# Kernel optimization log

Hardware: AMD Instinct MI355X
Metric: run time of the kernel (lower is better)

The kernel has to match this reference:

```python
import jax, jax.numpy as jnp
import numpy as np

B, T, C, H = 4, 2048, 1024, 16
HD = C // H  # head_dim = 64


def setup_inputs() -> dict:
    key = jax.random.key(0)
    k1, k2, k3 = jax.random.split(key, 3)
    x = jax.random.normal(k1, (B, T, C), dtype=jnp.float32)
    # nn.Linear weights are [out, in]; we store transposed [in, out] for x @ W
    w_qkv = jax.random.normal(k2, (C, 3 * C), dtype=jnp.float32) * (1.0 / np.sqrt(C))
    w_proj = jax.random.normal(k3, (C, C), dtype=jnp.float32) * (1.0 / np.sqrt(C))
    return {"x": x, "w_qkv": w_qkv, "w_proj": w_proj}


def reference(x, w_qkv, w_proj):
    Bs, Ts, Cs = x.shape
    qkv = x @ w_qkv  # [B,T,3C]
    q, k, v = jnp.split(qkv, 3, axis=-1)

    def split_heads(t):
        return t.reshape(Bs, Ts, H, HD).transpose(0, 2, 1, 3)  # [B,H,T,HD]

    q, k, v = split_heads(q), split_heads(k), split_heads(v)
    scale = 1.0 / np.sqrt(HD)
    scores = jnp.einsum('bhqd,bhkd->bhqk', q, k) * scale  # [B,H,T,T]
    causal = jnp.tril(jnp.ones((Ts, Ts), dtype=bool))
    scores = jnp.where(causal, scores, -jnp.inf)
    weights = jax.nn.softmax(scores, axis=-1)
    out = jnp.einsum('bhqk,bhkd->bhqd', weights, v)  # [B,H,T,HD]
    out = out.transpose(0, 2, 1, 3).reshape(Bs, Ts, Cs)
    return out @ w_proj
```

## Files before the change

kernel.cpp:

```cpp
#include <hip/hip_runtime.h>
#include <stdint.h>


typedef __attribute__((ext_vector_type(8))) short bf16x8;
typedef __attribute__((ext_vector_type(4))) float f32x4;

#define MFMA(a, b, c) __builtin_amdgcn_mfma_f32_16x16x32_bf16((a), (b), (c), 0, 0, 0)

#define NB 4
#define NT 2048
#define NC 1024
#define NH 16
#define HD 64
#define SCALE_Q 0.18033688011112042f

__device__ __forceinline__ short f2bf(float f) {
  union { float fv; uint32_t u; } v; v.fv = f;
  uint32_t u = v.u;
  uint32_t r = (u + 0x7fffu + ((u >> 16) & 1u)) >> 16;
  return (short)(r & 0xffffu);
}

__device__ __forceinline__ void gl_lds16(const void* g, void* l) {
  __builtin_amdgcn_global_load_lds(
      (const __attribute__((address_space(1))) void*)g,
      (__attribute__((address_space(3))) void*)l, 16, 0, 0);
}


__global__ void cast_f32_bf16(const float* __restrict__ src, short* __restrict__ dst, int n8) {
  int i = blockIdx.x * blockDim.x + threadIdx.x;
  if (i >= n8) return;
  const float4* s4 = (const float4*)src;
  float4 a = s4[2 * i], b = s4[2 * i + 1];
  bf16x8 o;
  o[0] = f2bf(a.x); o[1] = f2bf(a.y); o[2] = f2bf(a.z); o[3] = f2bf(a.w);
  o[4] = f2bf(b.x); o[5] = f2bf(b.y); o[6] = f2bf(b.z); o[7] = f2bf(b.w);
  *(bf16x8*)&dst[8 * i] = o;
}

__global__ void transpose_cast(const float* __restrict__ src, short* __restrict__ dst,
                               int R, int Cc) {
  __shared__ float tile[64][65];
  int tid = threadIdx.x;
  int c0 = blockIdx.x * 64;
  int r0 = blockIdx.y * 64;
  int lr = tid >> 4;
  int lc = (tid & 15) * 4;
#pragma unroll
  for (int i = 0; i < 4; i++) {
    int rr = lr + i * 16;
    float4 v = *(const float4*)&src[(size_t)(r0 + rr) * Cc + c0 + lc];
    tile[rr][lc + 0] = v.x; tile[rr][lc + 1] = v.y;
    tile[rr][lc + 2] = v.z; tile[rr][lc + 3] = v.w;
  }
  __syncthreads();
  int oc = tid >> 2;
  int seg = (tid & 3) * 16;
  bf16x8 o0, o1;
#pragma unroll
  for (int u = 0; u < 8; u++) o0[u] = f2bf(tile[seg + u][oc]);
#pragma unroll
  for (int u = 0; u < 8; u++) o1[u] = f2bf(tile[seg + 8 + u][oc]);
  size_t base = (size_t)(c0 + oc) * R + r0 + seg;
  *(bf16x8*)&dst[base] = o0;
  *(bf16x8*)&dst[base + 8] = o1;
}


__global__ __launch_bounds__(256, 2)
void gemm_bt_kernel(const short* __restrict__ A, const short* __restrict__ BT,
                    int N, int K, int mode,
                    short* __restrict__ q, short* __restrict__ kk, short* __restrict__ vT,
                    float* __restrict__ f_out) {
  __shared__ short sA[128 * 32];
  __shared__ short sB[128 * 32];
  const int tid = threadIdx.x;
  const int lane = tid & 63;
  const int w = tid >> 6;
  const int quad = lane >> 4;
  const int r = lane & 15;
  const int bn0 = blockIdx.x * 128;
  const int bm0 = blockIdx.y * 128;
  const int wm = (w >> 1) * 64;
  const int wn = (w & 1) * 64;

  f32x4 acc[4][4];
#pragma unroll
  for (int i = 0; i < 4; i++)
#pragma unroll
    for (int j = 0; j < 4; j++) acc[i][j] = (f32x4){0.f, 0.f, 0.f, 0.f};

  for (int kb = 0; kb < K; kb += 32) {
    __syncthreads();
#pragma unroll
    for (int rnd = 0; rnd < 2; rnd++) {
      int ci = rnd * 256 + tid;
      int m = ci >> 2, inner = ci & 3;
      const char* ga = (const char*)(A + (size_t)(bm0 + m) * K + kb) + inner * 16;
      gl_lds16(ga, (char*)sA + ci * 16);
      const char* gb = (const char*)(BT + (size_t)(bn0 + m) * K + kb) + inner * 16;
      gl_lds16(gb, (char*)sB + ci * 16);
    }
    __syncthreads();
    bf16x8 af[4], bfr[4];
#pragma unroll
    for (int i = 0; i < 4; i++) {
      af[i]  = *(const bf16x8*)&sA[(wm + i * 16 + r) * 32 + quad * 8];
      bfr[i] = *(const bf16x8*)&sB[(wn + i * 16 + r) * 32 + quad * 8];
    }
#pragma unroll
    for (int i = 0; i < 4; i++)
#pragma unroll
      for (int j = 0; j < 4; j++)
        acc[i][j] = MFMA(af[i], bfr[j], acc[i][j]);
  }

  if (mode == 0) {
#pragma unroll
    for (int i = 0; i < 4; i++) {
      int mbase = bm0 + wm + i * 16 + quad * 4;
#pragma unroll
      for (int j = 0; j < 4; j++) {
        int n = bn0 + wn + j * 16 + r;
        int sel = n >> 10, rem = n & 1023, h = rem >> 6, d = rem & 63;
#pragma unroll
        for (int reg = 0; reg < 4; reg++) {
          int m = mbase + reg;
          int b = m >> 11, t = m & 2047;
          int bh = b * NH + h;
          float v = acc[i][j][reg];
          if (sel == 0) {
            q[((size_t)bh * NT + t) * HD + d] = f2bf(v * SCALE_Q);
          } else if (sel == 1) {
            kk[((size_t)bh * NT + t) * HD + d] = f2bf(v);
          } else {
            vT[((size_t)bh * HD + d) * NT + t] = f2bf(v);
          }
        }
      }
    }
  } else {
#pragma unroll
    for (int i = 0; i < 4; i++)
#pragma unroll
      for (int j = 0; j < 4; j++) {
        int n = bn0 + wn + j * 16 + r;
#pragma unroll
        for (int reg = 0; reg < 4; reg++) {
          int m = bm0 + wm + i * 16 + quad * 4 + reg;
          f_out[(size_t)m * N + n] = acc[i][j][reg];
        }
      }
  }
}


__global__ __launch_bounds__(256, 3)
void attn_kernel(const short* __restrict__ Q, const short* __restrict__ Kg,
                 const short* __restrict__ VT, short* __restrict__ Og) {
  __shared__ short sK[128 * 64];
  __shared__ short sV[64 * 128];
  __shared__ short sP[4][16 * 136];
  const int tid = threadIdx.x;
  const int lane = tid & 63;
  const int w = tid >> 6;
  const int quad = lane >> 4;
  const int r = lane & 15;

  const int n = blockIdx.x;
  const int xcd = n & 7;
  const int slot = n >> 3;
  const int bh = xcd * 8 + (slot & 7);
  const int band = 15 - (slot >> 3);
  const int ntile = band + 1;

  const short* Qb  = Q  + (size_t)bh * NT * HD;
  const short* Kb  = Kg + (size_t)bh * NT * HD;
  const short* VTb = VT + (size_t)bh * HD * NT;

  const int q0 = band * 128 + w * 32;

  bf16x8 bQ[2][2];
#pragma unroll
  for (int mi = 0; mi < 2; mi++) {
    const size_t qrow = ((size_t)q0 + mi * 16 + r) * HD;
    bQ[mi][0] = *(const bf16x8*)&Qb[qrow + quad * 8];
    bQ[mi][1] = *(const bf16x8*)&Qb[qrow + 32 + quad * 8];
  }
  bf16x8 vone;
#pragma unroll
  for (int u = 0; u < 8; u++) vone[u] = (short)0x3F80;

  f32x4 acc[2][4];
  f32x4 lacc[2];
#pragma unroll
  for (int mi = 0; mi < 2; mi++) {
    lacc[mi] = (f32x4){0.f, 0.f, 0.f, 0.f};
#pragma unroll
    for (int dt = 0; dt < 4; dt++) acc[mi][dt] = (f32x4){0.f, 0.f, 0.f, 0.f};
  }

  for (int kt = 0; kt < ntile; kt++) {
    const int kv0 = kt * 128;
    const bool diag = (kt == band);
    __syncthreads();
#pragma unroll
    for (int j = 0; j < 4; j++) {
      int idx = (w * 4 + j) * 64 + lane;
      int krow = idx >> 3, kch = idx & 7;
      int kg = kch ^ (krow & 7);
      gl_lds16(Kb + (size_t)(kv0 + krow) * HD + kg * 8, (char*)sK + idx * 16);
      int vrow = idx >> 4, vch = idx & 15;
      int vg = (vch & 8) | ((vch ^ vrow) & 7);
      gl_lds16(VTb + (size_t)vrow * NT + kv0 + vg * 8, (char*)sV + idx * 16);
    }
    __syncthreads();

    bf16x8 vf[4][4];
#pragma unroll
    for (int dt = 0; dt < 4; dt++)
#pragma unroll
      for (int c = 0; c < 4; c++) {
        int ch = quad + 4 * c;
        int sw = (ch & 8) | ((ch ^ (r & 7)) & 7);
        vf[dt][c] = *(const bf16x8*)&sV[(dt * 16 + r) * 128 + sw * 8];
      }

#pragma unroll
    for (int mi = 0; mi < 2; mi++) {
      const int nts = diag ? (w * 2 + mi + 1) : 8;
#pragma unroll
      for (int nt = 0; nt < 8; nt++) {
        uint32_t pk0 = 0, pk1 = 0;
        if (nt < nts) {
          const int krow = nt * 16 + r;
          const int sw0 = quad ^ (r & 7);
          bf16x8 k0 = *(const bf16x8*)&sK[krow * 64 + sw0 * 8];
          bf16x8 k1 = *(const bf16x8*)&sK[krow * 64 + (sw0 ^ 4) * 8];
          f32x4 st = (f32x4){0.f, 0.f, 0.f, 0.f};
          st = MFMA(k0, bQ[mi][0], st);
          st = MFMA(k1, bQ[mi][1], st);
          if (diag && nt == nts - 1) {
            const int kvb = kv0 + nt * 16 + quad * 4;
            const int qg = q0 + mi * 16 + r;
#pragma unroll
            for (int reg = 0; reg < 4; reg++)
              if (kvb + reg > qg) st[reg] = -1e30f;
          }
          uint32_t b0 = (uint16_t)f2bf(__builtin_amdgcn_exp2f(st[0]));
          uint32_t b1 = (uint16_t)f2bf(__builtin_amdgcn_exp2f(st[1]));
          uint32_t b2 = (uint16_t)f2bf(__builtin_amdgcn_exp2f(st[2]));
          uint32_t b3 = (uint16_t)f2bf(__builtin_amdgcn_exp2f(st[3]));
          pk0 = b0 | (b1 << 16);
          pk1 = b2 | (b3 << 16);
        }
        *(uint2*)&sP[w][r * 136 + nt * 16 + quad * 4] = make_uint2(pk0, pk1);
      }
      __builtin_amdgcn_s_waitcnt(0xc07f);
      bf16x8 aP[4];
#pragma unroll
      for (int c = 0; c < 4; c++)
        aP[c] = *(const bf16x8*)&sP[w][r * 136 + c * 32 + quad * 8];
#pragma unroll
      for (int c = 0; c < 4; c++)
        lacc[mi] = MFMA(aP[c], vone, lacc[mi]);
#pragma unroll
      for (int dt = 0; dt < 4; dt++)
#pragma unroll
        for (int c = 0; c < 4; c++)
          acc[mi][dt] = MFMA(aP[c], vf[dt][c], acc[mi][dt]);
    }
  }

  const int b = bh >> 4, h = bh & 15;
#pragma unroll
  for (int mi = 0; mi < 2; mi++)
#pragma unroll
    for (int reg = 0; reg < 4; reg++) {
      const int trow = q0 + mi * 16 + quad * 4 + reg;
      const float inv = 1.0f / lacc[mi][reg];
      const size_t base = ((size_t)(b * NT + trow)) * NC + h * HD;
#pragma unroll
      for (int dt = 0; dt < 4; dt++)
        Og[base + dt * 16 + r] = f2bf(acc[mi][dt][reg] * inv);
    }
}


extern "C" void kernel_launch(void* const* d_in, const int* in_sizes, int n_in,
                              void* d_out, int out_size, void* d_ws, size_t ws_size,
                              hipStream_t stream) {
  const float* x     = (const float*)d_in[0];
  const float* wqkv  = (const float*)d_in[1];
  const float* wproj = (const float*)d_in[2];
  float* out = (float*)d_out;

  char* ws = (char*)d_ws;
  short* xb  = (short*)(ws + 0);
  short* wqT = (short*)(ws + 16777216);
  short* wpT = (short*)(ws + 23068672);
  short* q   = (short*)(ws + 25165824);
  short* kk  = (short*)(ws + 41943040);
  short* vT  = (short*)(ws + 58720256);
  short* att = (short*)(ws + 75497472);

  cast_f32_bf16<<<4096, 256, 0, stream>>>(x, xb, (NB * NT * NC) / 8);
  transpose_cast<<<dim3(48, 16), 256, 0, stream>>>(wqkv, wqT, NC, 3 * NC);
  transpose_cast<<<dim3(16, 16), 256, 0, stream>>>(wproj, wpT, NC, NC);
  gemm_bt_kernel<<<dim3(24, 64), 256, 0, stream>>>(xb, wqT, 3 * NC, NC, 0, q, kk, vT, nullptr);
  attn_kernel<<<1024, 256, 0, stream>>>(q, kk, vT, att);
  gemm_bt_kernel<<<dim3(8, 64), 256, 0, stream>>>(att, wpT, NC, NC, 1, nullptr, nullptr, nullptr, out);
}
```

Before: 291.4 us.

## Rework GEMM: K=64 tiles, XOR-swizzled LDS, XCD-aware block mapping, vectorized epilogue

The GEMM kernel now stages 64-wide K slices with an XOR-swizzled LDS layout to avoid bank conflicts and halve the barrier count. A 1D grid is remapped so each XCD handles contiguous M rows for better L2 reuse. For q, k and the output projection, MFMA operands are swapped so each lane holds 4 consecutive columns, which allows packed vector stores instead of scalar scattered stores. LDS use doubles, which may lower occupancy.

Result: faster. 259.5 us (-11.0%).

```diff
diff --git a/kernel.cpp b/kernel.cpp
--- a/kernel.cpp
+++ b/kernel.cpp
@@ -70,20 +70,28 @@
 
 __global__ __launch_bounds__(256, 2)
 void gemm_bt_kernel(const short* __restrict__ A, const short* __restrict__ BT,
-                    int N, int K, int mode,
+                    int N, int K, int nbx, int mode,
                     short* __restrict__ q, short* __restrict__ kk, short* __restrict__ vT,
                     float* __restrict__ f_out) {
-  __shared__ short sA[128 * 32];
-  __shared__ short sB[128 * 32];
+  __shared__ short sA[128 * 64];
+  __shared__ short sB[128 * 64];
   const int tid = threadIdx.x;
   const int lane = tid & 63;
   const int w = tid >> 6;
   const int quad = lane >> 4;
   const int r = lane & 15;
-  const int bn0 = blockIdx.x * 128;
-  const int bm0 = blockIdx.y * 128;
+
+  const int bid = blockIdx.x;
+  const int xcd = bid & 7;
+  const int local = bid >> 3;
+  const int mloc = local / nbx, nloc = local - mloc * nbx;
+  const int bm0 = (xcd * 8 + mloc) * 128;
+  const int bn0 = nloc * 128;
+
   const int wm = (w >> 1) * 64;
   const int wn = (w & 1) * 64;
+  const int sel = (mode == 0) ? (bn0 >> 10) : 3;
+  const bool swapped = (sel != 2);
 
   f32x4 acc[4][4];
 #pragma unroll
@@ -91,67 +99,83 @@
 #pragma unroll
     for (int j = 0; j < 4; j++) acc[i][j] = (f32x4){0.f, 0.f, 0.f, 0.f};
 
-  for (int kb = 0; kb < K; kb += 32) {
+  for (int kb = 0; kb < K; kb += 64) {
     __syncthreads();
 #pragma unroll
-    for (int rnd = 0; rnd < 2; rnd++) {
-      int ci = rnd * 256 + tid;
-      int m = ci >> 2, inner = ci & 3;
-      const char* ga = (const char*)(A + (size_t)(bm0 + m) * K + kb) + inner * 16;
-      gl_lds16(ga, (char*)sA + ci * 16);
-      const char* gb = (const char*)(BT + (size_t)(bn0 + m) * K + kb) + inner * 16;
-      gl_lds16(gb, (char*)sB + ci * 16);
+    for (int j2 = 0; j2 < 4; j2++) {
+      int idx = (w * 4 + j2) * 64 + lane;
+      int row = idx >> 3, ch = idx & 7;
+      int g = ch ^ (row & 7);
+      gl_lds16(A + (size_t)(bm0 + row) * K + kb + g * 8, (char*)sA + idx * 16);
+      gl_lds16(BT + (size_t)(bn0 + row) * K + kb + g * 8, (char*)sB + idx * 16);
     }
     __syncthreads();
-    bf16x8 af[4], bfr[4];
+#pragma unroll
+    for (int c = 0; c < 2; c++) {
+      bf16x8 af[4], bfr[4];
+#pragma unroll
+      for (int i = 0; i < 4; i++) {
+        const int sw = ((c << 2) + quad) ^ (r & 7);
+        af[i]  = *(const bf16x8*)&sA[(wm + i * 16 + r) * 64 + sw * 8];
+        bfr[i] = *(const bf16x8*)&sB[(wn + i * 16 + r) * 64 + sw * 8];
+      }
+      if (swapped) {
+#pragma unroll
+        for (int i = 0; i < 4; i++)
+#pragma unroll
+          for (int j = 0; j < 4; j++)
+            acc[i][j] = MFMA(bfr[j], af[i], acc[i][j]);
+      } else {
+#pragma unroll
+        for (int i = 0; i < 4; i++)
+#pragma unroll
+          for (int j = 0; j < 4; j++)
+            acc[i][j] = MFMA(af[i], bfr[j], acc[i][j]);
+      }
+    }
+  }
+
+  if (mode == 1) {
 #pragma unroll
     for (int i = 0; i < 4; i++) {
-      af[i]  = *(const bf16x8*)&sA[(wm + i * 16 + r) * 32 + quad * 8];
-      bfr[i] = *(const bf16x8*)&sB[(wn + i * 16 + r) * 32 + quad * 8];
-    }
-#pragma unroll
-    for (int i = 0; i < 4; i++)
-#pragma unroll
-      for (int j = 0; j < 4; j++)
-        acc[i][j] = MFMA(af[i], bfr[j], acc[i][j]);
-  }
-
-  if (mode == 0) {
+      const int m = bm0 + wm + i * 16 + r;
+#pragma unroll
+      for (int j = 0; j < 4; j++) {
+        const int nf = bn0 + wn + j * 16 + quad * 4;
+        *(f32x4*)&f_out[(size_t)m * N + nf] = acc[i][j];
+      }
+    }
+  } else if (sel == 2) {
+#pragma unroll
+    for (int j = 0; j < 4; j++) {
+      const int n = bn0 + wn + j * 16 + r;
+      const int d = n & 63, h = (n & 1023) >> 6;
+#pragma unroll
+      for (int i = 0; i < 4; i++) {
+        const int t0 = bm0 + wm + i * 16 + quad * 4;
+        const int bh = (t0 >> 11) * NH + h;
+        uint32_t p0 = (uint16_t)f2bf(acc[i][j][0]) | ((uint32_t)(uint16_t)f2bf(acc[i][j][1]) << 16);
+        uint32_t p1 = (uint16_t)f2bf(acc[i][j][2]) | ((uint32_t)(uint16_t)f2bf(acc[i][j][3]) << 16);
+        *(uint2*)&vT[((size_t)bh * HD + d) * NT + (t0 & 2047)] = make_uint2(p0, p1);
+      }
+    }
+  } else {
+    short* dst = (sel == 0) ? q : kk;
+    const float scl = (sel == 0) ? SCALE_Q : 1.0f;
 #pragma unroll
     for (int i = 0; i < 4; i++) {
-      int mbase = bm0 + wm + i * 16 + quad * 4;
+      const int t = bm0 + wm + i * 16 + r;
+      const int bb = (t >> 11) * NH;
+      const int tt = t & 2047;
 #pragma unroll
       for (int j = 0; j < 4; j++) {
-        int n = bn0 + wn + j * 16 + r;
-        int sel = n >> 10, rem = n & 1023, h = rem >> 6, d = rem & 63;
-#pragma unroll
-        for (int reg = 0; reg < 4; reg++) {
-          int m = mbase + reg;
-          int b = m >> 11, t = m & 2047;
-          int bh = b * NH + h;
-          float v = acc[i][j][reg];
-          if (sel == 0) {
-            q[((size_t)bh * NT + t) * HD + d] = f2bf(v * SCALE_Q);
-          } else if (sel == 1) {
-            kk[((size_t)bh * NT + t) * HD + d] = f2bf(v);
-          } else {
-            vT[((size_t)bh * HD + d) * NT + t] = f2bf(v);
-          }
-        }
-      }
-    }
-  } else {
-#pragma unroll
-    for (int i = 0; i < 4; i++)
-#pragma unroll
-      for (int j = 0; j < 4; j++) {
-        int n = bn0 + wn + j * 16 + r;
-#pragma unroll
-        for (int reg = 0; reg < 4; reg++) {
-          int m = bm0 + wm + i * 16 + quad * 4 + reg;
-          f_out[(size_t)m * N + n] = acc[i][j][reg];
-        }
-      }
+        const int nf = bn0 + wn + j * 16 + quad * 4;
+        const int rem = nf & 1023, h = rem >> 6, d0 = rem & 63;
+        uint32_t p0 = (uint16_t)f2bf(acc[i][j][0] * scl) | ((uint32_t)(uint16_t)f2bf(acc[i][j][1] * scl) << 16);
+        uint32_t p1 = (uint16_t)f2bf(acc[i][j][2] * scl) | ((uint32_t)(uint16_t)f2bf(acc[i][j][3] * scl) << 16);
+        *(uint2*)&dst[((size_t)(bb + h) * NT + tt) * HD + d0] = make_uint2(p0, p1);
+      }
+    }
   }
 }
 
@@ -308,7 +332,7 @@
   cast_f32_bf16<<<4096, 256, 0, stream>>>(x, xb, (NB * NT * NC) / 8);
   transpose_cast<<<dim3(48, 16), 256, 0, stream>>>(wqkv, wqT, NC, 3 * NC);
   transpose_cast<<<dim3(16, 16), 256, 0, stream>>>(wproj, wpT, NC, NC);
-  gemm_bt_kernel<<<dim3(24, 64), 256, 0, stream>>>(xb, wqT, 3 * NC, NC, 0, q, kk, vT, nullptr);
+  gemm_bt_kernel<<<1536, 256, 0, stream>>>(xb, wqT, 3 * NC, NC, 24, 0, q, kk, vT, nullptr);
   attn_kernel<<<1024, 256, 0, stream>>>(q, kk, vT, att);
-  gemm_bt_kernel<<<dim3(8, 64), 256, 0, stream>>>(att, wpT, NC, NC, 1, nullptr, nullptr, nullptr, out);
-}
+  gemm_bt_kernel<<<512, 256, 0, stream>>>(att, wpT, NC, NC, 8, 1, nullptr, nullptr, nullptr, out);
+}
```
